# Kernel optimization log

Measured on AMD Instinct MI355X. Metric: run time of the kernel, lower is better.

Reference implementation:

```python
import jax, jax.numpy as jnp
import numpy as np

D_MODEL = 1024
N_HEADS = 16
D_HEAD = D_MODEL // N_HEADS
SCALE = 1.0 / float(np.sqrt(D_HEAD))


def setup_inputs() -> dict:
    key = jax.random.key(0)
    ks = jax.random.split(key, 6)
    B, T = 4, 2048
    x = jax.random.normal(ks[0], (B, T, D_MODEL), dtype=jnp.float32)
    # torch Linear weights are [out, in]; y = x @ W.T
    s = 1.0 / np.sqrt(D_MODEL)
    Wq = jax.random.uniform(ks[1], (D_MODEL, D_MODEL), jnp.float32, -s, s)
    Wk = jax.random.uniform(ks[2], (D_MODEL, D_MODEL), jnp.float32, -s, s)
    Wv = jax.random.uniform(ks[3], (D_MODEL, D_MODEL), jnp.float32, -s, s)
    Wo = jax.random.uniform(ks[4], (D_MODEL, D_MODEL), jnp.float32, -s, s)
    bo = jax.random.uniform(ks[5], (D_MODEL,), jnp.float32, -s, s)
    return {"x": x, "Wq": Wq, "Wk": Wk, "Wv": Wv, "Wo": Wo, "bo": bo}


def reference(x, Wq, Wk, Wv, Wo, bo):
    B, T, D = x.shape
    # QKV projections (torch Linear: x @ W.T), split into heads -> [B, H, T, d]
    def heads(y):
        return y.reshape(B, T, N_HEADS, D_HEAD).transpose(0, 2, 1, 3)
    q = heads(x @ Wq.T)
    k = heads(x @ Wk.T)
    v = heads(x @ Wv.T)
    scores = jnp.einsum("bhqd,bhkd->bhqk", q, k) * SCALE  # [B,H,T,T]
    probs = jax.nn.softmax(scores, axis=-1)
    # dropout is identity in eval/inference mode
    out = jnp.einsum("bhqk,bhkd->bhqd", probs, v)  # [B,H,T,d]
    out = out.transpose(0, 2, 1, 3).reshape(B, T, D)
    return out @ Wo.T + bo
```

## Files before the change

kernel.cpp:

```cpp
#include <hip/hip_runtime.h>
#include <stdint.h>

#define D_MODEL 1024
#define NH 16
#define DH 64
#define TSEQ 2048
#define BATCH 4
#define MTOT (BATCH*TSEQ)
#define NQ (MTOT*D_MODEL)
#define WSZ (D_MODEL*D_MODEL)
#define QSCALE 0.18033688f

typedef __attribute__((ext_vector_type(8))) short bf16x8;
typedef __attribute__((ext_vector_type(8))) unsigned short u16x8;
typedef __attribute__((ext_vector_type(4))) float f32x4;
typedef __attribute__((ext_vector_type(2))) float f32x2;
typedef unsigned short u16;
typedef unsigned int u32;

__device__ __forceinline__ void gl_lds16(const void* g, void* l) {
  __builtin_amdgcn_global_load_lds(
      (__attribute__((address_space(1))) void*)g,
      (__attribute__((address_space(3))) void*)l, 16, 0, 0);
}
__device__ __forceinline__ u16 f2bf(float f) {
  u32 u = __builtin_bit_cast(u32, f);
  u = u + 0x7fffu + ((u >> 16) & 1u);
  return (u16)(u >> 16);
}
__device__ __forceinline__ float bf2f(u16 b) {
  u32 u = ((u32)b) << 16;
  return __builtin_bit_cast(float, u);
}

__device__ __forceinline__ void exp2pk4(const f32x4 s, float& e0, float& e1,
                                        float& e2, float& e3, u32& pk01,
                                        u32& pk23) {
  asm("v_exp_f32 %0, %6\n\t"
      "v_exp_f32 %1, %7\n\t"
      "v_exp_f32 %2, %8\n\t"
      "v_exp_f32 %3, %9\n\t"
      "s_nop 1\n\t"
      "v_cvt_pk_bf16_f32 %4, %0, %1\n\t"
      "v_cvt_pk_bf16_f32 %5, %2, %3"
      : "=&v"(e0), "=&v"(e1), "=&v"(e2), "=&v"(e3), "=&v"(pk01), "=&v"(pk23)
      : "v"(s[0]), "v"(s[1]), "v"(s[2]), "v"(s[3]));
}

__global__ __launch_bounds__(256) void detect_dtype(
    const u32* __restrict__ wq_raw, int* __restrict__ flag)
{
  __shared__ int cnt;
  if (threadIdx.x == 0) cnt = 0;
  __syncthreads();
  int c = 0;
  for (int i = threadIdx.x; i < 2048; i += 256) {
    const u32 e = (wq_raw[i] >> 7) & 0xFFu;
    if (e >= 90u && e <= 126u) ++c;
  }
  atomicAdd(&cnt, c);
  __syncthreads();
  if (threadIdx.x == 0) *flag = (cnt > 1024) ? 1 : 0;
}

__global__ __launch_bounds__(256) void convert_inputs(
    const void* __restrict__ x, const void* __restrict__ wq,
    const void* __restrict__ wk, const void* __restrict__ wv,
    const void* __restrict__ wo,
    u16* __restrict__ xb, u16* __restrict__ wqb, u16* __restrict__ wkb,
    u16* __restrict__ wvb, u16* __restrict__ wob,
    const int* __restrict__ flag_p)
{
  if (*flag_p) return;
  const int seg = blockIdx.y;
  const void* src; u16* dst; int n;
  switch (seg) {
    case 0:  src = x;  dst = xb;  n = NQ;  break;
    case 1:  src = wq; dst = wqb; n = WSZ; break;
    case 2:  src = wk; dst = wkb; n = WSZ; break;
    case 3:  src = wv; dst = wvb; n = WSZ; break;
    default: src = wo; dst = wob; n = WSZ; break;
  }
  const int idx = (blockIdx.x * 256 + threadIdx.x) * 8;
  if (idx >= n) return;
  const float4 f0 = *(const float4*)((const float*)src + idx);
  const float4 f1 = *(const float4*)((const float*)src + idx + 4);
  union { u16 s[8]; u16x8 v; } u;
  u.s[0] = f2bf(f0.x); u.s[1] = f2bf(f0.y); u.s[2] = f2bf(f0.z); u.s[3] = f2bf(f0.w);
  u.s[4] = f2bf(f1.x); u.s[5] = f2bf(f1.y); u.s[6] = f2bf(f1.z); u.s[7] = f2bf(f1.w);
  *(u16x8*)(dst + idx) = u.v;
}

__global__ __launch_bounds__(256) void qkv_gemm(
    const int* __restrict__ flag_p, const u16* __restrict__ x_raw,
    u16* __restrict__ dout,
    const u16* __restrict__ Wq, const u16* __restrict__ Wk,
    const u16* __restrict__ Wv,
    const void* __restrict__ wq_r, const void* __restrict__ wk_r,
    const void* __restrict__ wv_r,
    u16* __restrict__ Ko, u16* __restrict__ VTo)
{
  __shared__ __align__(16) u16 As[2 * 128 * 32];
  __shared__ __align__(16) u16 Bs[2 * 128 * 32];
  const int flag = *flag_p;
  const u16* __restrict__ X = flag ? x_raw : dout;
  u16* __restrict__ QTo = flag ? dout : dout + NQ;
  const int t = threadIdx.x;
  const int z = blockIdx.z;
  const u16* __restrict__ Wc = (z == 0) ? Wq : (z == 1) ? Wk : Wv;
  const u16* __restrict__ Wr = (const u16*)((z == 0) ? wq_r : (z == 1) ? wk_r : wv_r);
  const u16* __restrict__ W = flag ? Wr : Wc;
  const int bx = blockIdx.x;
  const int mb = ((bx & 7) << 3) | (bx >> 3);
  const int m0 = mb * 128;
  const int n0 = blockIdx.y * 128;
  const int wave = t >> 6, lane = t & 63;
  const int wm = (wave >> 1) * 64, wn = (wave & 1) * 64;
  const int lr = lane & 15, kg = (lane >> 4) * 8;

  const int srow0 = t >> 2, skc = (t & 3) * 8;
  const int srow1 = srow0 + 64;
  const u16* a0 = X + (size_t)(m0 + srow0) * D_MODEL + skc;
  const u16* a1 = X + (size_t)(m0 + srow1) * D_MODEL + skc;
  const u16* b0 = W + (size_t)(n0 + srow0) * D_MODEL + skc;
  const u16* b1 = W + (size_t)(n0 + srow1) * D_MODEL + skc;

  f32x4 acc[4][4] = {};

  for (int kt = 0; kt < D_MODEL / 64; ++kt) {
    gl_lds16(a0,      &As[t * 8]);
    gl_lds16(a1,      &As[(t + 256) * 8]);
    gl_lds16(a0 + 32, &As[4096 + t * 8]);
    gl_lds16(a1 + 32, &As[4096 + (t + 256) * 8]);
    gl_lds16(b0,      &Bs[t * 8]);
    gl_lds16(b1,      &Bs[(t + 256) * 8]);
    gl_lds16(b0 + 32, &Bs[4096 + t * 8]);
    gl_lds16(b1 + 32, &Bs[4096 + (t + 256) * 8]);
    a0 += 64; a1 += 64; b0 += 64; b1 += 64;
    __syncthreads();
#pragma unroll
    for (int h = 0; h < 2; ++h) {
      bf16x8 af[4], bfr[4];
#pragma unroll
      for (int i = 0; i < 4; ++i)
        af[i] = *(const bf16x8*)&As[h * 4096 + (wm + i * 16 + lr) * 32 + kg];
#pragma unroll
      for (int j = 0; j < 4; ++j)
        bfr[j] = *(const bf16x8*)&Bs[h * 4096 + (wn + j * 16 + lr) * 32 + kg];
#pragma unroll
      for (int i = 0; i < 4; ++i)
#pragma unroll
        for (int j = 0; j < 4; ++j)
          acc[i][j] = __builtin_amdgcn_mfma_f32_16x16x32_bf16(af[i], bfr[j], acc[i][j], 0, 0, 0);
    }
    __syncthreads();
  }

  const int bidx = m0 >> 11;
  if (z == 1) {
#pragma unroll
    for (int i = 0; i < 4; ++i) {
      const int rowg = m0 + wm + i * 16 + ((lane >> 4) << 2);
      const int tq = rowg & (TSEQ - 1);
#pragma unroll
      for (int j = 0; j < 4; ++j) {
        const int colg = n0 + wn + j * 16 + lr;
        const int h = colg >> 6, d = colg & 63;
        u16* dst = Ko + ((size_t)(bidx * NH + h) * TSEQ + tq) * DH + d;
#pragma unroll
        for (int r = 0; r < 4; ++r)
          dst[(size_t)r * DH] = f2bf(acc[i][j][r]);
      }
    }
  } else {
    u16* O = (z == 0) ? QTo : VTo;
    const float sc = (z == 0) ? QSCALE : 1.0f;
#pragma unroll
    for (int i = 0; i < 4; ++i) {
      const int rowg = m0 + wm + i * 16 + ((lane >> 4) << 2);
      const int tq = rowg & (TSEQ - 1);
#pragma unroll
      for (int j = 0; j < 4; ++j) {
        const int colg = n0 + wn + j * 16 + lr;
        const int h = colg >> 6, d = colg & 63;
        union { u16 s[4]; uint2 v; } u;
#pragma unroll
        for (int r = 0; r < 4; ++r) u.s[r] = f2bf(acc[i][j][r] * sc);
        *(uint2*)&O[((size_t)(bidx * NH + h) * DH + d) * TSEQ + tq] = u.v;
      }
    }
  }
}

__global__ __launch_bounds__(256) void flash_attn(
    const int* __restrict__ flag_p, const u16* __restrict__ dout,
    const u16* __restrict__ K, const u16* __restrict__ VT,
    u16* __restrict__ AO)
{
  __shared__ __align__(16) u16 Ks[2][2 * 64 * 32];
  __shared__ __align__(16) u16 Vs[2][2 * 64 * 32];
  __shared__ __align__(16) u16 Ps[4 * 64 * 72];
  __shared__ float Ls[4 * 64];
  const int flag = *flag_p;
  const u16* __restrict__ QT = flag ? dout : dout + NQ;
  const int t = threadIdx.x;
  const int wave = t >> 6, lane = t & 63;
  const int lr = lane & 15, g = lane >> 4, kg = g * 8;
  const int bh = blockIdx.x;
  const int q0 = blockIdx.y * 256;
  const u16* __restrict__ QTh = QT + (size_t)bh * DH * TSEQ;
  const u16* __restrict__ Kh = K + (size_t)bh * TSEQ * DH;
  const u16* __restrict__ Vh = VT + (size_t)bh * DH * TSEQ;

  const int qi = q0 + wave * 64 + lr;
  bf16x8 qf[8];
#pragma unroll
  for (int s = 0; s < 4; ++s) {
    union { u16 v[8]; bf16x8 b; } u0, u1;
#pragma unroll
    for (int j = 0; j < 8; ++j) {
      u0.v[j] = QTh[(size_t)(kg + j) * TSEQ + qi + s * 16];
      u1.v[j] = QTh[(size_t)(32 + kg + j) * TSEQ + qi + s * 16];
    }
    qf[s * 2] = u0.b; qf[s * 2 + 1] = u1.b;
  }

  f32x4 acc[4][4] = {};
  f32x2 ls0[4] = {}, ls1[4] = {};

  const int srow = t >> 2, skc = (t & 3) * 8;
  const u16* kb = Kh + (size_t)srow * DH + skc;
  const u16* vb = Vh + (size_t)srow * TSEQ + skc;
  u16* const pw = &Ps[wave * 64 * 72];

  gl_lds16(kb,      &Ks[0][t * 8]);
  gl_lds16(kb + 32, &Ks[0][(t + 256) * 8]);
  gl_lds16(vb,      &Vs[0][t * 8]);
  gl_lds16(vb + 32, &Vs[0][(t + 256) * 8]);
  kb += 64 * DH; vb += 64;

  int cur = 0;
  for (int j0 = 0; j0 < TSEQ; j0 += 64) {
    __syncthreads();
    if (j0 + 64 < TSEQ) {
      gl_lds16(kb,      &Ks[cur ^ 1][t * 8]);
      gl_lds16(kb + 32, &Ks[cur ^ 1][(t + 256) * 8]);
      gl_lds16(vb,      &Vs[cur ^ 1][t * 8]);
      gl_lds16(vb + 32, &Vs[cur ^ 1][(t + 256) * 8]);
      kb += 64 * DH; vb += 64;
    }
    const u16* __restrict__ Kc = Ks[cur];
    const u16* __restrict__ Vc = Vs[cur];

#pragma unroll
    for (int jn = 0; jn < 2; ++jn) {
      const bf16x8 kf0 = *(const bf16x8*)&Kc[(jn * 16 + lr) * 32 + kg];
      const bf16x8 kf1 = *(const bf16x8*)&Kc[2048 + (jn * 16 + lr) * 32 + kg];
#pragma unroll
      for (int s = 0; s < 4; ++s) {
        f32x4 sS = {};
        sS = __builtin_amdgcn_mfma_f32_16x16x32_bf16(kf0, qf[s * 2],     sS, 0, 0, 0);
        sS = __builtin_amdgcn_mfma_f32_16x16x32_bf16(kf1, qf[s * 2 + 1], sS, 0, 0, 0);
        float e0, e1, e2, e3;
        uint2 w;
        exp2pk4(sS, e0, e1, e2, e3, w.x, w.y);
        ls0[s] += (f32x2){e0, e1};
        ls1[s] += (f32x2){e2, e3};
        *(uint2*)&pw[s * 16 * 72 + lr * 72 + jn * 16 + g * 4] = w;
      }
    }

    bf16x8 pf0[4];
#pragma unroll
    for (int s = 0; s < 4; ++s)
      pf0[s] = *(const bf16x8*)&pw[s * 16 * 72 + lr * 72 + kg];

#pragma unroll
    for (int jn = 2; jn < 4; ++jn) {
      const bf16x8 kf0 = *(const bf16x8*)&Kc[(jn * 16 + lr) * 32 + kg];
      const bf16x8 kf1 = *(const bf16x8*)&Kc[2048 + (jn * 16 + lr) * 32 + kg];
#pragma unroll
      for (int s = 0; s < 4; ++s) {
        f32x4 sS = {};
        sS = __builtin_amdgcn_mfma_f32_16x16x32_bf16(kf0, qf[s * 2],     sS, 0, 0, 0);
        sS = __builtin_amdgcn_mfma_f32_16x16x32_bf16(kf1, qf[s * 2 + 1], sS, 0, 0, 0);
        float e0, e1, e2, e3;
        uint2 w;
        exp2pk4(sS, e0, e1, e2, e3, w.x, w.y);
        ls0[s] += (f32x2){e0, e1};
        ls1[s] += (f32x2){e2, e3};
        *(uint2*)&pw[s * 16 * 72 + lr * 72 + jn * 16 + g * 4] = w;
      }
    }

#pragma unroll
    for (int dn = 0; dn < 4; ++dn) {
      const bf16x8 vf0 = *(const bf16x8*)&Vc[(dn * 16 + lr) * 32 + kg];
#pragma unroll
      for (int s = 0; s < 4; ++s)
        acc[s][dn] = __builtin_amdgcn_mfma_f32_16x16x32_bf16(pf0[s], vf0, acc[s][dn], 0, 0, 0);
    }

    bf16x8 pf1[4];
#pragma unroll
    for (int s = 0; s < 4; ++s)
      pf1[s] = *(const bf16x8*)&pw[s * 16 * 72 + lr * 72 + 32 + kg];
#pragma unroll
    for (int dn = 0; dn < 4; ++dn) {
      const bf16x8 vf1 = *(const bf16x8*)&Vc[2048 + (dn * 16 + lr) * 32 + kg];
#pragma unroll
      for (int s = 0; s < 4; ++s)
        acc[s][dn] = __builtin_amdgcn_mfma_f32_16x16x32_bf16(pf1[s], vf1, acc[s][dn], 0, 0, 0);
    }
    cur ^= 1;
  }

#pragma unroll
  for (int s = 0; s < 4; ++s) {
    float l = (ls0[s][0] + ls0[s][1]) + (ls1[s][0] + ls1[s][1]);
    l += __shfl_xor(l, 16, 64);
    l += __shfl_xor(l, 32, 64);
    Ls[wave * 64 + s * 16 + lr] = l;
  }
  __syncthreads();

  const int bb = bh >> 4, hh = bh & 15;
#pragma unroll
  for (int s = 0; s < 4; ++s) {
#pragma unroll
    for (int r = 0; r < 4; ++r) {
      const int qq = g * 4 + r;
      const float inv = 1.f / fmaxf(Ls[wave * 64 + s * 16 + qq], 1e-30f);
      const int ti = q0 + wave * 64 + s * 16 + qq;
      u16* dst = AO + (((size_t)bb * TSEQ + ti) * NH + hh) * DH + lr;
#pragma unroll
      for (int dn = 0; dn < 4; ++dn)
        dst[dn * 16] = f2bf(acc[s][dn][r] * inv);
    }
  }
}

__global__ __launch_bounds__(256) void out_gemm(
    const int* __restrict__ flag_p,
    const u16* __restrict__ A, const u16* __restrict__ W,
    const void* __restrict__ wo_r,
    const void* __restrict__ bias_raw, void* __restrict__ outp)
{
  __shared__ __align__(16) u16 As[2 * 128 * 32];
  __shared__ __align__(16) u16 Bs[2 * 128 * 32];
  const int flag = *flag_p;
  const u16* __restrict__ Wm = flag ? (const u16*)wo_r : W;
  const int t = threadIdx.x;
  const int bx = blockIdx.x;
  const int mb = ((bx & 7) << 3) | (bx >> 3);
  const int m0 = mb * 128;
  const int n0 = blockIdx.y * 128;
  const int wave = t >> 6, lane = t & 63;
  const int wm = (wave >> 1) * 64, wn = (wave & 1) * 64;
  const int lr = lane & 15, kg = (lane >> 4) * 8;

  const int srow0 = t >> 2, skc = (t & 3) * 8;
  const int srow1 = srow0 + 64;
  const u16* a0 = A + (size_t)(m0 + srow0) * D_MODEL + skc;
  const u16* a1 = A + (size_t)(m0 + srow1) * D_MODEL + skc;
  const u16* b0 = Wm + (size_t)(n0 + srow0) * D_MODEL + skc;
  const u16* b1 = Wm + (size_t)(n0 + srow1) * D_MODEL + skc;

  f32x4 acc[4][4] = {};

  for (int kt = 0; kt < D_MODEL / 64; ++kt) {
    gl_lds16(a0,      &As[t * 8]);
    gl_lds16(a1,      &As[(t + 256) * 8]);
    gl_lds16(a0 + 32, &As[4096 + t * 8]);
    gl_lds16(a1 + 32, &As[4096 + (t + 256) * 8]);
    gl_lds16(b0,      &Bs[t * 8]);
    gl_lds16(b1,      &Bs[(t + 256) * 8]);
    gl_lds16(b0 + 32, &Bs[4096 + t * 8]);
    gl_lds16(b1 + 32, &Bs[4096 + (t + 256) * 8]);
    a0 += 64; a1 += 64; b0 += 64; b1 += 64;
    __syncthreads();
#pragma unroll
    for (int h = 0; h < 2; ++h) {
      bf16x8 af[4], bfr[4];
#pragma unroll
      for (int i = 0; i < 4; ++i)
        af[i] = *(const bf16x8*)&As[h * 4096 + (wm + i * 16 + lr) * 32 + kg];
#pragma unroll
      for (int j = 0; j < 4; ++j)
        bfr[j] = *(const bf16x8*)&Bs[h * 4096 + (wn + j * 16 + lr) * 32 + kg];
#pragma unroll
      for (int i = 0; i < 4; ++i)
#pragma unroll
        for (int j = 0; j < 4; ++j)
          acc[i][j] = __builtin_amdgcn_mfma_f32_16x16x32_bf16(af[i], bfr[j], acc[i][j], 0, 0, 0);
    }
    __syncthreads();
  }

#pragma unroll
  for (int j = 0; j < 4; ++j) {
    const int colg = n0 + wn + j * 16 + lr;
    const float bv = flag ? bf2f(((const u16*)bias_raw)[colg])
                          : ((const float*)bias_raw)[colg];
#pragma unroll
    for (int i = 0; i < 4; ++i) {
      const int rowg = m0 + wm + i * 16 + ((lane >> 4) << 2);
      if (flag) {
        u16* dst = (u16*)outp + (size_t)rowg * D_MODEL + colg;
#pragma unroll
        for (int r = 0; r < 4; ++r)
          dst[(size_t)r * D_MODEL] = f2bf(acc[i][j][r] + bv);
      } else {
        float* dst = (float*)outp + (size_t)rowg * D_MODEL + colg;
#pragma unroll
        for (int r = 0; r < 4; ++r)
          dst[(size_t)r * D_MODEL] = acc[i][j][r] + bv;
      }
    }
  }
}

extern "C" void kernel_launch(void* const* d_in, const int* in_sizes, int n_in,
                              void* d_out, int out_size, void* d_ws, size_t ws_size,
                              hipStream_t stream) {
  const void* x  = d_in[0];
  const void* wq = d_in[1];
  const void* wk = d_in[2];
  const void* wv = d_in[3];
  const void* wo = d_in[4];
  const void* bo = d_in[5];
  u16* dout = (u16*)d_out;

  int* flag = (int*)d_ws;
  u16* wqb = (u16*)d_ws + 8;
  u16* wkb = wqb + WSZ;
  u16* wvb = wkb + WSZ;
  u16* wob = wvb + WSZ;
  u16* kk  = wob + WSZ;
  u16* vt  = kk + NQ;
  u16* ao  = vt + NQ;

  detect_dtype<<<1, 256, 0, stream>>>((const u32*)wq, flag);

  dim3 gc(NQ / (256 * 8), 5);
  convert_inputs<<<gc, dim3(256), 0, stream>>>(
      x, wq, wk, wv, wo, dout, wqb, wkb, wvb, wob, flag);

  dim3 g1(MTOT / 128, D_MODEL / 128, 3);
  qkv_gemm<<<g1, dim3(256), 0, stream>>>(
      flag, (const u16*)x, dout, wqb, wkb, wvb, wq, wk, wv, kk, vt);

  dim3 g2(BATCH * NH, TSEQ / 256, 1);
  flash_attn<<<g2, dim3(256), 0, stream>>>(flag, dout, kk, vt, ao);

  dim3 g3(MTOT / 128, D_MODEL / 128, 1);
  out_gemm<<<g3, dim3(256), 0, stream>>>(flag, ao, wob, wo, bo, d_out);
}
```

Baseline: 287.7 us.

## Fuse Q, K, V projections into one block sharing the X tile

The QKV GEMM now computes Q, K and V in a single block, loading each X tile into LDS once and reusing it against three weight tiles, instead of launching three z-slices that each reload X. K is computed transposed (B operand as A) so its output can be written with vectorized 8-byte stores rather than scalar stores. The block-index swizzle for L2 locality is removed from both GEMMs. The cost is three times the accumulator registers (48 f32x4), more LDS per block and a third as many blocks, which lowers occupancy and parallelism.

After: 268.3 us. -6.7%, faster.

```diff
diff --git a/kernel.cpp b/kernel.cpp
--- a/kernel.cpp
+++ b/kernel.cpp
@@ -91,7 +91,7 @@
   *(u16x8*)(dst + idx) = u.v;
 }
 
-__global__ __launch_bounds__(256) void qkv_gemm(
+__global__ __launch_bounds__(256, 2) void qkv_gemm(
     const int* __restrict__ flag_p, const u16* __restrict__ x_raw,
     u16* __restrict__ dout,
     const u16* __restrict__ Wq, const u16* __restrict__ Wk,
@@ -100,43 +100,57 @@
     const void* __restrict__ wv_r,
     u16* __restrict__ Ko, u16* __restrict__ VTo)
 {
-  __shared__ __align__(16) u16 As[2 * 128 * 32];
-  __shared__ __align__(16) u16 Bs[2 * 128 * 32];
+  __shared__ __align__(16) u16 As [2 * 128 * 32];
+  __shared__ __align__(16) u16 Bqs[2 * 128 * 32];
+  __shared__ __align__(16) u16 Bks[2 * 128 * 32];
+  __shared__ __align__(16) u16 Bvs[2 * 128 * 32];
   const int flag = *flag_p;
-  const u16* __restrict__ X = flag ? x_raw : dout;
+  const u16* __restrict__ X  = flag ? x_raw : dout;
   u16* __restrict__ QTo = flag ? dout : dout + NQ;
+  const u16* __restrict__ WQ = flag ? (const u16*)wq_r : Wq;
+  const u16* __restrict__ WK = flag ? (const u16*)wk_r : Wk;
+  const u16* __restrict__ WV = flag ? (const u16*)wv_r : Wv;
   const int t = threadIdx.x;
-  const int z = blockIdx.z;
-  const u16* __restrict__ Wc = (z == 0) ? Wq : (z == 1) ? Wk : Wv;
-  const u16* __restrict__ Wr = (const u16*)((z == 0) ? wq_r : (z == 1) ? wk_r : wv_r);
-  const u16* __restrict__ W = flag ? Wr : Wc;
-  const int bx = blockIdx.x;
-  const int mb = ((bx & 7) << 3) | (bx >> 3);
-  const int m0 = mb * 128;
+  const int m0 = blockIdx.x * 128;
   const int n0 = blockIdx.y * 128;
   const int wave = t >> 6, lane = t & 63;
   const int wm = (wave >> 1) * 64, wn = (wave & 1) * 64;
-  const int lr = lane & 15, kg = (lane >> 4) * 8;
+  const int lr = lane & 15, g = lane >> 4, kg = g * 8;
 
   const int srow0 = t >> 2, skc = (t & 3) * 8;
   const int srow1 = srow0 + 64;
-  const u16* a0 = X + (size_t)(m0 + srow0) * D_MODEL + skc;
-  const u16* a1 = X + (size_t)(m0 + srow1) * D_MODEL + skc;
-  const u16* b0 = W + (size_t)(n0 + srow0) * D_MODEL + skc;
-  const u16* b1 = W + (size_t)(n0 + srow1) * D_MODEL + skc;
-
-  f32x4 acc[4][4] = {};
+  const u16* a0 = X  + (size_t)(m0 + srow0) * D_MODEL + skc;
+  const u16* a1 = X  + (size_t)(m0 + srow1) * D_MODEL + skc;
+  const u16* q0p = WQ + (size_t)(n0 + srow0) * D_MODEL + skc;
+  const u16* q1p = WQ + (size_t)(n0 + srow1) * D_MODEL + skc;
+  const u16* k0p = WK + (size_t)(n0 + srow0) * D_MODEL + skc;
+  const u16* k1p = WK + (size_t)(n0 + srow1) * D_MODEL + skc;
+  const u16* v0p = WV + (size_t)(n0 + srow0) * D_MODEL + skc;
+  const u16* v1p = WV + (size_t)(n0 + srow1) * D_MODEL + skc;
+
+  f32x4 accq[4][4] = {};
+  f32x4 acck[4][4] = {};
+  f32x4 accv[4][4] = {};
 
   for (int kt = 0; kt < D_MODEL / 64; ++kt) {
-    gl_lds16(a0,      &As[t * 8]);
-    gl_lds16(a1,      &As[(t + 256) * 8]);
-    gl_lds16(a0 + 32, &As[4096 + t * 8]);
-    gl_lds16(a1 + 32, &As[4096 + (t + 256) * 8]);
-    gl_lds16(b0,      &Bs[t * 8]);
-    gl_lds16(b1,      &Bs[(t + 256) * 8]);
-    gl_lds16(b0 + 32, &Bs[4096 + t * 8]);
-    gl_lds16(b1 + 32, &Bs[4096 + (t + 256) * 8]);
-    a0 += 64; a1 += 64; b0 += 64; b1 += 64;
+    gl_lds16(a0,       &As [t * 8]);
+    gl_lds16(a1,       &As [(t + 256) * 8]);
+    gl_lds16(a0 + 32,  &As [4096 + t * 8]);
+    gl_lds16(a1 + 32,  &As [4096 + (t + 256) * 8]);
+    gl_lds16(q0p,      &Bqs[t * 8]);
+    gl_lds16(q1p,      &Bqs[(t + 256) * 8]);
+    gl_lds16(q0p + 32, &Bqs[4096 + t * 8]);
+    gl_lds16(q1p + 32, &Bqs[4096 + (t + 256) * 8]);
+    gl_lds16(k0p,      &Bks[t * 8]);
+    gl_lds16(k1p,      &Bks[(t + 256) * 8]);
+    gl_lds16(k0p + 32, &Bks[4096 + t * 8]);
+    gl_lds16(k1p + 32, &Bks[4096 + (t + 256) * 8]);
+    gl_lds16(v0p,      &Bvs[t * 8]);
+    gl_lds16(v1p,      &Bvs[(t + 256) * 8]);
+    gl_lds16(v0p + 32, &Bvs[4096 + t * 8]);
+    gl_lds16(v1p + 32, &Bvs[4096 + (t + 256) * 8]);
+    a0 += 64; a1 += 64; q0p += 64; q1p += 64;
+    k0p += 64; k1p += 64; v0p += 64; v1p += 64;
     __syncthreads();
 #pragma unroll
     for (int h = 0; h < 2; ++h) {
@@ -146,48 +160,65 @@
         af[i] = *(const bf16x8*)&As[h * 4096 + (wm + i * 16 + lr) * 32 + kg];
 #pragma unroll
       for (int j = 0; j < 4; ++j)
-        bfr[j] = *(const bf16x8*)&Bs[h * 4096 + (wn + j * 16 + lr) * 32 + kg];
+        bfr[j] = *(const bf16x8*)&Bqs[h * 4096 + (wn + j * 16 + lr) * 32 + kg];
 #pragma unroll
       for (int i = 0; i < 4; ++i)
 #pragma unroll
         for (int j = 0; j < 4; ++j)
-          acc[i][j] = __builtin_amdgcn_mfma_f32_16x16x32_bf16(af[i], bfr[j], acc[i][j], 0, 0, 0);
+          accq[i][j] = __builtin_amdgcn_mfma_f32_16x16x32_bf16(af[i], bfr[j], accq[i][j], 0, 0, 0);
+#pragma unroll
+      for (int j = 0; j < 4; ++j)
+        bfr[j] = *(const bf16x8*)&Bks[h * 4096 + (wn + j * 16 + lr) * 32 + kg];
+#pragma unroll
+      for (int j = 0; j < 4; ++j)
+#pragma unroll
+        for (int i = 0; i < 4; ++i)
+          acck[j][i] = __builtin_amdgcn_mfma_f32_16x16x32_bf16(bfr[j], af[i], acck[j][i], 0, 0, 0);
+#pragma unroll
+      for (int j = 0; j < 4; ++j)
+        bfr[j] = *(const bf16x8*)&Bvs[h * 4096 + (wn + j * 16 + lr) * 32 + kg];
+#pragma unroll
+      for (int i = 0; i < 4; ++i)
+#pragma unroll
+        for (int j = 0; j < 4; ++j)
+          accv[i][j] = __builtin_amdgcn_mfma_f32_16x16x32_bf16(af[i], bfr[j], accv[i][j], 0, 0, 0);
     }
     __syncthreads();
   }
 
   const int bidx = m0 >> 11;
-  if (z == 1) {
+#pragma unroll
+  for (int zz = 0; zz < 2; ++zz) {
+    u16* O = zz ? VTo : QTo;
+    const float sc = zz ? 1.0f : QSCALE;
 #pragma unroll
     for (int i = 0; i < 4; ++i) {
-      const int rowg = m0 + wm + i * 16 + ((lane >> 4) << 2);
+      const int rowg = m0 + wm + i * 16 + (g << 2);
       const int tq = rowg & (TSEQ - 1);
 #pragma unroll
       for (int j = 0; j < 4; ++j) {
         const int colg = n0 + wn + j * 16 + lr;
         const int h = colg >> 6, d = colg & 63;
-        u16* dst = Ko + ((size_t)(bidx * NH + h) * TSEQ + tq) * DH + d;
-#pragma unroll
-        for (int r = 0; r < 4; ++r)
-          dst[(size_t)r * DH] = f2bf(acc[i][j][r]);
-      }
-    }
-  } else {
-    u16* O = (z == 0) ? QTo : VTo;
-    const float sc = (z == 0) ? QSCALE : 1.0f;
-#pragma unroll
-    for (int i = 0; i < 4; ++i) {
-      const int rowg = m0 + wm + i * 16 + ((lane >> 4) << 2);
-      const int tq = rowg & (TSEQ - 1);
-#pragma unroll
-      for (int j = 0; j < 4; ++j) {
-        const int colg = n0 + wn + j * 16 + lr;
-        const int h = colg >> 6, d = colg & 63;
+        const f32x4 a = zz ? accv[i][j] : accq[i][j];
         union { u16 s[4]; uint2 v; } u;
 #pragma unroll
-        for (int r = 0; r < 4; ++r) u.s[r] = f2bf(acc[i][j][r] * sc);
+        for (int r = 0; r < 4; ++r) u.s[r] = f2bf(a[r] * sc);
         *(uint2*)&O[((size_t)(bidx * NH + h) * DH + d) * TSEQ + tq] = u.v;
       }
+    }
+  }
+#pragma unroll
+  for (int j = 0; j < 4; ++j) {
+    const int dg = n0 + wn + j * 16 + (g << 2);
+    const int hh = dg >> 6, d0 = dg & 63;
+#pragma unroll
+    for (int i = 0; i < 4; ++i) {
+      const int tg = m0 + wm + i * 16 + lr;
+      const int tq = tg & (TSEQ - 1);
+      union { u16 s[4]; uint2 v; } u;
+#pragma unroll
+      for (int r = 0; r < 4; ++r) u.s[r] = f2bf(acck[j][i][r]);
+      *(uint2*)&Ko[((size_t)(bidx * NH + hh) * TSEQ + tq) * DH + d0] = u.v;
     }
   }
 }
@@ -351,9 +382,7 @@
   const int flag = *flag_p;
   const u16* __restrict__ Wm = flag ? (const u16*)wo_r : W;
   const int t = threadIdx.x;
-  const int bx = blockIdx.x;
-  const int mb = ((bx & 7) << 3) | (bx >> 3);
-  const int m0 = mb * 128;
+  const int m0 = blockIdx.x * 128;
   const int n0 = blockIdx.y * 128;
   const int wave = t >> 6, lane = t & 63;
   const int wm = (wave >> 1) * 64, wn = (wave & 1) * 64;
@@ -446,7 +475,7 @@
   convert_inputs<<<gc, dim3(256), 0, stream>>>(
       x, wq, wk, wv, wo, dout, wqb, wkb, wvb, wob, flag);
 
-  dim3 g1(MTOT / 128, D_MODEL / 128, 3);
+  dim3 g1(MTOT / 128, D_MODEL / 128, 1);
   qkv_gemm<<<g1, dim3(256), 0, stream>>>(
       flag, (const u16*)x, dout, wqb, wkb, wvb, wq, wk, wv, kk, vt);
 
```
